# Optimization experiments

Hardware: AMD Instinct MI355X
Metric: run time of the kernel (lower is better)

Reference implementation:

```python
import jax, jax.numpy as jnp
import numpy as np

B, N, D = 32, 512, 256
ITERATION_STEPS = 2


def setup_inputs() -> dict:
    key = jax.random.key(0)
    ks = jax.random.split(key, 20)
    node = jax.random.normal(ks[0], (B, N, D), dtype=jnp.float32)
    node_mask = jnp.ones((B, N), dtype=jnp.int32)
    graphs = [(jax.random.uniform(ks[1 + i], (B, N, N)) < 0.05).astype(jnp.int32)
              for i in range(6)]
    s = 0.02
    params = {
        'w_nw': jax.random.normal(ks[8], (D, 1)) * s,
        'b_nw': jnp.zeros((1,), jnp.float32),
        'w_self': jax.random.normal(ks[9], (D, D)) * s,
        'b_self': jnp.zeros((D,), jnp.float32),
        'w_arg1': jax.random.normal(ks[10], (D, D)) * s,
        'w_arg2': jax.random.normal(ks[11], (D, D)) * s,
        'w_arg3': jax.random.normal(ks[12], (D, D)) * s,
        'w_arg4': jax.random.normal(ks[13], (D, D)) * s,
        'w_punct': jax.random.normal(ks[14], (D, D)) * s,
        'w_punct_re': jax.random.normal(ks[15], (D, D)) * s,
    }
    return {'node': node, 'node_mask': node_mask,
            'arg_graph_1': graphs[0], 'arg_graph_2': graphs[1],
            'arg_graph_3': graphs[2], 'arg_graph_4': graphs[3],
            'punct_graph': graphs[4], 'punct_graph_re': graphs[5],
            **params}


def reference(node, node_mask, arg_graph_1, arg_graph_2, arg_graph_3, arg_graph_4,
              punct_graph, punct_graph_re,
              w_nw, b_nw, w_self, b_self,
              w_arg1, w_arg2, w_arg3, w_arg4, w_punct, w_punct_re):
    n = node.shape[1]
    diag = jnp.eye(n, dtype=node_mask.dtype)  # [N,N]
    # dd_graph: pairwise valid mask with zeroed diagonal, [B,N,N]
    dd = node_mask[:, None, :] * node_mask[:, :, None] * (1 - diag)
    G = jnp.stack([arg_graph_1, arg_graph_2, arg_graph_3, arg_graph_4,
                   punct_graph, punct_graph_re], 0) * dd[None]  # [6,B,N,N]
    Gf = G.astype(node.dtype)
    # neighbor count over all 6 edge types; replace 0 by 1 to avoid div-by-zero
    nn_num = Gf.sum(axis=(0, -1))  # [B,N]
    nn_num = jnp.where(nn_num >= 1, nn_num, jnp.ones_like(nn_num))
    W = jnp.stack([w_arg1, w_arg2, w_arg3, w_arg4, w_punct, w_punct_re], 0)  # [6,D,D]

    all_weight = []
    for _ in range(ITERATION_STEPS):
        # (1) node relatedness measure
        d_node_weight = jax.nn.sigmoid(node @ w_nw + b_nw)[..., 0]  # [B,N]
        all_weight.append(d_node_weight)
        self_node_info = node @ w_self + b_self  # [B,N,D]
        # (2) message propagation: per edge type k, project then aggregate
        proj = jnp.einsum('bnd,kde->kbne', node, W)            # [6,B,N,D]
        masked_w = d_node_weight[None, :, None, :] * Gf        # [6,B,N,N]
        agg = jnp.einsum('kbmn,kbne->bme', masked_w, proj)     # [B,N,D]
        # (3) update
        node = jax.nn.relu(self_node_info + agg / nn_num[..., None])
    return node, jnp.stack(all_weight, axis=1)  # [B,N,D], [B,steps,N]
```

## Files before the change

kernel.cpp:

```cpp
#include <hip/hip_runtime.h>

#define Bb 32
#define Nn 512
#define Dd 256
#define KC 1792

typedef __bf16 bf16x8 __attribute__((ext_vector_type(8)));
typedef float  f32x4  __attribute__((ext_vector_type(4)));
typedef unsigned short u16;

__device__ __forceinline__ u16 f2bf(float x){
  union { float f; unsigned u; } c; c.f = x;
  unsigned u = c.u;
  u += 0x7FFFu + ((u >> 16) & 1u);
  return (u16)(u >> 16);
}

__global__ __launch_bounds__(256) void k_prep(
    const float* __restrict__ wself,
    const float* __restrict__ w0, const float* __restrict__ w1,
    const float* __restrict__ w2, const float* __restrict__ w3,
    const float* __restrict__ w4, const float* __restrict__ w5,
    u16* __restrict__ wcatT){
  int e = blockIdx.x;
  const float* Ws[7] = {wself, w0, w1, w2, w3, w4, w5};
  for (int c = threadIdx.x; c < KC; c += 256){
    int g = c >> 8, j = c & 255;
    wcatT[(size_t)e*KC + c] = f2bf(Ws[g][j*Dd + e]);
  }
}

__global__ __launch_bounds__(256) void k_pack(
    const int* __restrict__ g0, const int* __restrict__ g1,
    const int* __restrict__ g2, const int* __restrict__ g3,
    const int* __restrict__ g4, const int* __restrict__ g5,
    const int* __restrict__ mask, unsigned* __restrict__ Gp,
    float* __restrict__ rs){
  int wid = threadIdx.x >> 6, l = threadIdx.x & 63;
  int r = blockIdx.x * 4 + wid;
  int b = r >> 9, m = r & 511;
  const int* gs[6] = {g0, g1, g2, g3, g4, g5};
  int mcol[8];
  #pragma unroll
  for (int h = 0; h < 8; ++h) mcol[h] = mask[b * Nn + h * 64 + l];
  int s = 0;
  #pragma unroll
  for (int k = 0; k < 6; ++k){
    const int* gp = gs[k] + (size_t)r * Nn;
    unsigned my = 0;
    #pragma unroll
    for (int h = 0; h < 8; ++h){
      int col = h * 64 + l;
      int v = gp[col];
      unsigned long long bal = __ballot(v && mcol[h] && col != m);
      s += __popcll(bal);
      if (l == 2 * h)     my = (unsigned)bal;
      if (l == 2 * h + 1) my = (unsigned)(bal >> 32);
    }
    if (l < 16) Gp[((size_t)k * Bb * Nn + r) * 16 + l] = my;
  }
  if (l == 0){
    int mm = mask[r];
    rs[r] = mm ? 1.0f / (float)(s < 1 ? 1 : s) : 0.0f;
  }
}

__global__ __launch_bounds__(256) void k_dw(
    const float* __restrict__ node, const int* __restrict__ mask,
    const float* __restrict__ wnw, const float* __restrict__ bnw,
    float* __restrict__ aw_out,
    u16* __restrict__ Z, u16* __restrict__ XT){
  __shared__ float tile[32][268];
  __shared__ float dws[32];
  int b = blockIdx.x >> 4, n0 = (blockIdx.x & 15) << 5;
  int t = threadIdx.x;
  int row = t >> 3, seg = t & 7;
  const float* src = node + ((size_t)(b * Nn + n0 + row)) * Dd + seg * 32;
  u16* zn = Z + ((size_t)(b * Nn + n0 + row)) * KC + seg * 32;
  #pragma unroll
  for (int c = 0; c < 8; ++c){
    float4 v = ((const float4*)src)[c];
    tile[row][seg * 32 + c * 4 + 0] = v.x;
    tile[row][seg * 32 + c * 4 + 1] = v.y;
    tile[row][seg * 32 + c * 4 + 2] = v.z;
    tile[row][seg * 32 + c * 4 + 3] = v.w;
    ushort4 h;
    h.x = f2bf(v.x); h.y = f2bf(v.y); h.z = f2bf(v.z); h.w = f2bf(v.w);
    ((ushort4*)zn)[c] = h;
  }
  __syncthreads();
  float s = 0.f;
  #pragma unroll
  for (int c = 0; c < 32; ++c) s += tile[row][seg * 32 + c] * wnw[seg * 32 + c];
  s += __shfl_xor(s, 1); s += __shfl_xor(s, 2); s += __shfl_xor(s, 4);
  if (seg == 0){
    float dw = 1.f / (1.f + expf(-(s + bnw[0])));
    aw_out[b * (2 * Nn) + n0 + row] = dw;
    dws[row] = mask[b * Nn + n0 + row] ? dw : 0.f;
  }
  __syncthreads();
  #pragma unroll
  for (int p = 0; p < 4; ++p){
    int d = p * 64 + (t >> 2);
    int j0 = (t & 3) * 8;
    union { u16 h[8]; uint4 v; } pk;
    #pragma unroll
    for (int jj = 0; jj < 8; ++jj)
      pk.h[jj] = f2bf(dws[j0 + jj] * tile[j0 + jj][d]);
    *(uint4*)(XT + ((size_t)(b * Dd + d)) * Nn + n0 + j0) = pk.v;
  }
}

__global__ __launch_bounds__(256) void k_agg(
    const unsigned* __restrict__ Gp,
    const u16* __restrict__ XT, const float* __restrict__ rs,
    u16* __restrict__ Z){
  int mt = blockIdx.x, b = blockIdx.y, kg = blockIdx.z;
  int m0 = mt * 64;
  const unsigned* Gr = Gp + ((size_t)kg * Bb * Nn + b * Nn + m0) * 16;
  const u16* Xb = XT + (size_t)b * Dd * Nn;
  __shared__ u16 As[64 * 72];
  __shared__ u16 Bs[256 * 72];
  int t = threadIdx.x, lane = t & 63, wn = t >> 6;
  int arow = t >> 2, aq = t & 3;
  unsigned wpre[8];
  #pragma unroll
  for (int ks = 0; ks < 8; ++ks)
    wpre[ks] = Gr[arow * 16 + ks * 2 + (aq >> 1)];

  f32x4 acc[4][4];
  #pragma unroll
  for (int i = 0; i < 4; ++i)
    #pragma unroll
    for (int q = 0; q < 4; ++q) acc[i][q] = (f32x4){0.f, 0.f, 0.f, 0.f};

  for (int ks = 0; ks < 8; ++ks){
    int k0 = ks * 64;
    {
      unsigned bits = (wpre[ks] >> ((aq & 1) * 16)) & 0xFFFFu;
      union { u16 h[16]; uint4 v[2]; } pk;
      #pragma unroll
      for (int c = 0; c < 16; ++c)
        pk.h[c] = ((bits >> c) & 1u) ? 0x3F80 : 0;
      *(uint4*)&As[arow * 72 + aq * 16]     = pk.v[0];
      *(uint4*)&As[arow * 72 + aq * 16 + 8] = pk.v[1];
    }
    #pragma unroll
    for (int p = 0; p < 8; ++p){
      int rowb = p * 32 + (t >> 3);
      *(uint4*)&Bs[rowb * 72 + (t & 7) * 8] =
          *(const uint4*)(Xb + (size_t)rowb * Nn + k0 + (t & 7) * 8);
    }
    __syncthreads();
    #pragma unroll
    for (int kk = 0; kk < 2; ++kk){
      bf16x8 av[4], bv[4];
      #pragma unroll
      for (int i = 0; i < 4; ++i)
        av[i] = *(const bf16x8*)&As[(i * 16 + (lane & 15)) * 72 + kk * 32 + (lane >> 4) * 8];
      #pragma unroll
      for (int q = 0; q < 4; ++q)
        bv[q] = *(const bf16x8*)&Bs[(wn * 64 + q * 16 + (lane & 15)) * 72 + kk * 32 + (lane >> 4) * 8];
      #pragma unroll
      for (int i = 0; i < 4; ++i)
        #pragma unroll
        for (int q = 0; q < 4; ++q)
          acc[i][q] = __builtin_amdgcn_mfma_f32_16x16x32_bf16(av[i], bv[q], acc[i][q], 0, 0, 0);
    }
    __syncthreads();
  }
  int kgcol = 256 + kg * 256 + wn * 64;
  #pragma unroll
  for (int i = 0; i < 4; ++i){
    #pragma unroll
    for (int r = 0; r < 4; ++r){
      int mg = m0 + i * 16 + (lane >> 4) * 4 + r;
      float sc = rs[b * Nn + mg];
      u16* zp = Z + ((size_t)(b * Nn + mg)) * KC + kgcol + (lane & 15);
      #pragma unroll
      for (int q = 0; q < 4; ++q)
        zp[q * 16] = f2bf(acc[i][q][r] * sc);
    }
  }
}

__global__ __launch_bounds__(256) void k_upd(
    const u16* __restrict__ Z, const u16* __restrict__ wcatT,
    const float* __restrict__ bself, float* __restrict__ outp){
  int n0 = blockIdx.x * 128, m0 = blockIdx.y * 128;
  __shared__ u16 As[128 * 72];
  __shared__ u16 Bs[128 * 72];
  int t = threadIdx.x, lane = t & 63, wid = t >> 6;
  int wm = wid >> 1, wn = wid & 1;
  f32x4 acc[4][4];
  #pragma unroll
  for (int i = 0; i < 4; ++i)
    #pragma unroll
    for (int q = 0; q < 4; ++q) acc[i][q] = (f32x4){0.f, 0.f, 0.f, 0.f};

  for (int ks = 0; ks < 28; ++ks){
    int k0 = ks * 64;
    #pragma unroll
    for (int p = 0; p < 4; ++p){
      int row = p * 32 + (t >> 3);
      *(uint4*)&As[row * 72 + (t & 7) * 8] =
          *(const uint4*)(Z + ((size_t)(m0 + row)) * KC + k0 + (t & 7) * 8);
      *(uint4*)&Bs[row * 72 + (t & 7) * 8] =
          *(const uint4*)(wcatT + ((size_t)(n0 + row)) * KC + k0 + (t & 7) * 8);
    }
    __syncthreads();
    #pragma unroll
    for (int kk = 0; kk < 2; ++kk){
      bf16x8 av[4], bv[4];
      #pragma unroll
      for (int i = 0; i < 4; ++i)
        av[i] = *(const bf16x8*)&As[(wm * 64 + i * 16 + (lane & 15)) * 72 + kk * 32 + (lane >> 4) * 8];
      #pragma unroll
      for (int q = 0; q < 4; ++q)
        bv[q] = *(const bf16x8*)&Bs[(wn * 64 + q * 16 + (lane & 15)) * 72 + kk * 32 + (lane >> 4) * 8];
      #pragma unroll
      for (int i = 0; i < 4; ++i)
        #pragma unroll
        for (int q = 0; q < 4; ++q)
          acc[i][q] = __builtin_amdgcn_mfma_f32_16x16x32_bf16(av[i], bv[q], acc[i][q], 0, 0, 0);
    }
    __syncthreads();
  }
  #pragma unroll
  for (int i = 0; i < 4; ++i){
    #pragma unroll
    for (int r = 0; r < 4; ++r){
      int mg = m0 + wm * 64 + i * 16 + (lane >> 4) * 4 + r;
      #pragma unroll
      for (int q = 0; q < 4; ++q){
        int e = n0 + wn * 64 + q * 16 + (lane & 15);
        float v = acc[i][q][r] + bself[e];
        outp[(size_t)mg * Dd + e] = v > 0.f ? v : 0.f;
      }
    }
  }
}

extern "C" void kernel_launch(void* const* d_in, const int* in_sizes, int n_in,
                              void* d_out, int out_size, void* d_ws, size_t ws_size,
                              hipStream_t stream){
  (void)in_sizes; (void)n_in; (void)out_size; (void)ws_size;
  const float* node  = (const float*)d_in[0];
  const int*   mask  = (const int*)d_in[1];
  const int*   g[6];
  for (int i = 0; i < 6; ++i) g[i] = (const int*)d_in[2 + i];
  const float* wnw   = (const float*)d_in[8];
  const float* bnw   = (const float*)d_in[9];
  const float* wself = (const float*)d_in[10];
  const float* bself = (const float*)d_in[11];
  const float* W[6];
  for (int i = 0; i < 6; ++i) W[i] = (const float*)d_in[12 + i];

  float* out_node = (float*)d_out;
  float* out_aw   = out_node + (size_t)Bb * Nn * Dd;

  char* ws = (char*)d_ws;
  u16*      wcatT = (u16*)(ws);
  float*    rs    = (float*)(ws + 917504);
  unsigned* Gp    = (unsigned*)(ws + 1048576);
  u16*      XT    = (u16*)(ws + 7340032);
  u16*      Z     = (u16*)(ws + 15728640);

  k_prep<<<256, 256, 0, stream>>>(wself, W[0], W[1], W[2], W[3], W[4], W[5], wcatT);
  k_pack<<<4096, 256, 0, stream>>>(g[0], g[1], g[2], g[3], g[4], g[5], mask, Gp, rs);

  for (int t = 0; t < 2; ++t){
    const float* nsrc = (t == 0) ? node : out_node;
    k_dw<<<512, 256, 0, stream>>>(nsrc, mask, wnw, bnw, out_aw + t * Nn, Z, XT);
    k_agg<<<dim3(8, 32, 6), 256, 0, stream>>>(Gp, XT, rs, Z);
    k_upd<<<dim3(2, 128), 256, 0, stream>>>(Z, wcatT, bself, out_node);
  }
}
```

Before: 288.9 us.

## Vectorize graph bit-packing with int4 loads and widen update GEMM tile to full D

The adjacency packing kernel now has each thread load int4 vectors from all six graphs and build 4-bit nibbles, replacing per-element loads and ballots. The nibbles are assembled into 32-bit words through shared memory, and the neighbour count is reduced with shuffles. This targets the memory-bound cost of reading six B×N×N int32 graphs. Separately, the update GEMM tile changes from 128x128 to 64x256, so each block covers the full output width and reads its Z rows once instead of twice, while loading a larger B tile per step.

```diff
diff --git a/kernel.cpp b/kernel.cpp
--- a/kernel.cpp
+++ b/kernel.cpp
@@ -36,32 +36,53 @@
     const int* __restrict__ g4, const int* __restrict__ g5,
     const int* __restrict__ mask, unsigned* __restrict__ Gp,
     float* __restrict__ rs){
-  int wid = threadIdx.x >> 6, l = threadIdx.x & 63;
-  int r = blockIdx.x * 4 + wid;
-  int b = r >> 9, m = r & 511;
-  const int* gs[6] = {g0, g1, g2, g3, g4, g5};
-  int mcol[8];
-  #pragma unroll
-  for (int h = 0; h < 8; ++h) mcol[h] = mask[b * Nn + h * 64 + l];
-  int s = 0;
-  #pragma unroll
-  for (int k = 0; k < 6; ++k){
-    const int* gp = gs[k] + (size_t)r * Nn;
-    unsigned my = 0;
-    #pragma unroll
-    for (int h = 0; h < 8; ++h){
-      int col = h * 64 + l;
-      int v = gp[col];
-      unsigned long long bal = __ballot(v && mcol[h] && col != m);
-      s += __popcll(bal);
-      if (l == 2 * h)     my = (unsigned)bal;
-      if (l == 2 * h + 1) my = (unsigned)(bal >> 32);
-    }
-    if (l < 16) Gp[((size_t)k * Bb * Nn + r) * 16 + l] = my;
-  }
-  if (l == 0){
-    int mm = mask[r];
-    rs[r] = mm ? 1.0f / (float)(s < 1 ? 1 : s) : 0.0f;
+  __shared__ unsigned char nibs[12][128];
+  __shared__ int reds[4];
+  int t = threadIdx.x;
+  int half = t >> 7, c = t & 127;
+  int R = blockIdx.x * 2;
+  int r = R + half, b = R >> 9, m = r & 511;
+
+  const int4* mrow4 = (const int4*)(mask + (size_t)b * Nn);
+  size_t gi = (size_t)r * 128 + c;
+  int4 mm  = mrow4[c];
+  int4 a0 = ((const int4*)g0)[gi];
+  int4 a1 = ((const int4*)g1)[gi];
+  int4 a2 = ((const int4*)g2)[gi];
+  int4 a3 = ((const int4*)g3)[gi];
+  int4 a4 = ((const int4*)g4)[gi];
+  int4 a5 = ((const int4*)g5)[gi];
+
+  unsigned dm = (c == (m >> 2)) ? (1u << (m & 3)) : 0u;
+  int stot = 0;
+#define DO_K(k, g)                                                         \
+  {                                                                        \
+    unsigned nib = (unsigned)((g.x & mm.x) | ((g.y & mm.y) << 1) |         \
+                              ((g.z & mm.z) << 2) | ((g.w & mm.w) << 3));  \
+    nib &= ~dm;                                                            \
+    stot += __popc(nib);                                                   \
+    nibs[k * 2 + half][c] = (unsigned char)nib;                           \
+  }
+  DO_K(0, a0) DO_K(1, a1) DO_K(2, a2) DO_K(3, a3) DO_K(4, a4) DO_K(5, a5)
+#undef DO_K
+
+  #pragma unroll
+  for (int off = 1; off < 64; off <<= 1) stot += __shfl_xor(stot, off);
+  if ((t & 63) == 0) reds[t >> 6] = stot;
+  __syncthreads();
+
+  if (t < 192){
+    int rg = t >> 4, w = t & 15;
+    int k = rg >> 1, h2 = rg & 1;
+    unsigned d0 = *(const unsigned*)&nibs[rg][w * 8];
+    unsigned d1 = *(const unsigned*)&nibs[rg][w * 8 + 4];
+    unsigned x0 = (d0 | (d0 >> 4)) & 0x00FF00FFu; x0 = (x0 | (x0 >> 8)) & 0xFFFFu;
+    unsigned x1 = (d1 | (d1 >> 4)) & 0x00FF00FFu; x1 = (x1 | (x1 >> 8)) & 0xFFFFu;
+    Gp[((size_t)k * Bb * Nn + (R + h2)) * 16 + w] = x0 | (x1 << 16);
+  } else if (t < 194){
+    int h2 = t - 192;
+    int s = reds[h2 * 2] + reds[h2 * 2 + 1];
+    rs[R + h2] = mask[R + h2] ? 1.0f / (float)(s < 1 ? 1 : s) : 0.0f;
   }
 }
 
@@ -187,53 +208,57 @@
 __global__ __launch_bounds__(256) void k_upd(
     const u16* __restrict__ Z, const u16* __restrict__ wcatT,
     const float* __restrict__ bself, float* __restrict__ outp){
-  int n0 = blockIdx.x * 128, m0 = blockIdx.y * 128;
-  __shared__ u16 As[128 * 72];
-  __shared__ u16 Bs[128 * 72];
+  int m0 = blockIdx.x * 64;
+  __shared__ u16 As[64 * 72];
+  __shared__ u16 Bs[256 * 72];
   int t = threadIdx.x, lane = t & 63, wid = t >> 6;
   int wm = wid >> 1, wn = wid & 1;
-  f32x4 acc[4][4];
-  #pragma unroll
-  for (int i = 0; i < 4; ++i)
-    #pragma unroll
-    for (int q = 0; q < 4; ++q) acc[i][q] = (f32x4){0.f, 0.f, 0.f, 0.f};
+  f32x4 acc[2][8];
+  #pragma unroll
+  for (int i = 0; i < 2; ++i)
+    #pragma unroll
+    for (int q = 0; q < 8; ++q) acc[i][q] = (f32x4){0.f, 0.f, 0.f, 0.f};
 
   for (int ks = 0; ks < 28; ++ks){
     int k0 = ks * 64;
     #pragma unroll
-    for (int p = 0; p < 4; ++p){
+    for (int p = 0; p < 2; ++p){
       int row = p * 32 + (t >> 3);
       *(uint4*)&As[row * 72 + (t & 7) * 8] =
           *(const uint4*)(Z + ((size_t)(m0 + row)) * KC + k0 + (t & 7) * 8);
+    }
+    #pragma unroll
+    for (int p = 0; p < 8; ++p){
+      int row = p * 32 + (t >> 3);
       *(uint4*)&Bs[row * 72 + (t & 7) * 8] =
-          *(const uint4*)(wcatT + ((size_t)(n0 + row)) * KC + k0 + (t & 7) * 8);
+          *(const uint4*)(wcatT + ((size_t)row) * KC + k0 + (t & 7) * 8);
     }
     __syncthreads();
     #pragma unroll
     for (int kk = 0; kk < 2; ++kk){
-      bf16x8 av[4], bv[4];
-      #pragma unroll
-      for (int i = 0; i < 4; ++i)
-        av[i] = *(const bf16x8*)&As[(wm * 64 + i * 16 + (lane & 15)) * 72 + kk * 32 + (lane >> 4) * 8];
-      #pragma unroll
-      for (int q = 0; q < 4; ++q)
-        bv[q] = *(const bf16x8*)&Bs[(wn * 64 + q * 16 + (lane & 15)) * 72 + kk * 32 + (lane >> 4) * 8];
-      #pragma unroll
-      for (int i = 0; i < 4; ++i)
+      bf16x8 av[2], bv[8];
+      #pragma unroll
+      for (int i = 0; i < 2; ++i)
+        av[i] = *(const bf16x8*)&As[(wm * 32 + i * 16 + (lane & 15)) * 72 + kk * 32 + (lane >> 4) * 8];
+      #pragma unroll
+      for (int q = 0; q < 8; ++q)
+        bv[q] = *(const bf16x8*)&Bs[(wn * 128 + q * 16 + (lane & 15)) * 72 + kk * 32 + (lane >> 4) * 8];
+      #pragma unroll
+      for (int i = 0; i < 2; ++i)
         #pragma unroll
-        for (int q = 0; q < 4; ++q)
+        for (int q = 0; q < 8; ++q)
           acc[i][q] = __builtin_amdgcn_mfma_f32_16x16x32_bf16(av[i], bv[q], acc[i][q], 0, 0, 0);
     }
     __syncthreads();
   }
   #pragma unroll
-  for (int i = 0; i < 4; ++i){
+  for (int i = 0; i < 2; ++i){
     #pragma unroll
     for (int r = 0; r < 4; ++r){
-      int mg = m0 + wm * 64 + i * 16 + (lane >> 4) * 4 + r;
-      #pragma unroll
-      for (int q = 0; q < 4; ++q){
-        int e = n0 + wn * 64 + q * 16 + (lane & 15);
+      int mg = m0 + wm * 32 + i * 16 + (lane >> 4) * 4 + r;
+      #pragma unroll
+      for (int q = 0; q < 8; ++q){
+        int e = wn * 128 + q * 16 + (lane & 15);
         float v = acc[i][q][r] + bself[e];
         outp[(size_t)mg * Dd + e] = v > 0.f ? v : 0.f;
       }
@@ -267,12 +292,12 @@
   u16*      Z     = (u16*)(ws + 15728640);
 
   k_prep<<<256, 256, 0, stream>>>(wself, W[0], W[1], W[2], W[3], W[4], W[5], wcatT);
-  k_pack<<<4096, 256, 0, stream>>>(g[0], g[1], g[2], g[3], g[4], g[5], mask, Gp, rs);
+  k_pack<<<8192, 256, 0, stream>>>(g[0], g[1], g[2], g[3], g[4], g[5], mask, Gp, rs);
 
   for (int t = 0; t < 2; ++t){
     const float* nsrc = (t == 0) ? node : out_node;
     k_dw<<<512, 256, 0, stream>>>(nsrc, mask, wnw, bnw, out_aw + t * Nn, Z, XT);
     k_agg<<<dim3(8, 32, 6), 256, 0, stream>>>(Gp, XT, rs, Z);
-    k_upd<<<dim3(2, 128), 256, 0, stream>>>(Z, wcatT, bself, out_node);
-  }
-}
+    k_upd<<<256, 256, 0, stream>>>(Z, wcatT, bself, out_node);
+  }
+}
```

Result: faster. 257.4 us (-10.9%).
